# Performance work log

Measured on AMD Instinct MI355X. Metric: run time of the kernel, lower is better.

The kernel has to match this reference:

```python
import jax, jax.numpy as jnp
import numpy as np

N_T = 256
N_LAT = 1024
N_INN = 512
N_G = 512
N_MU = 64
N_NEU = 1024  # MLP hidden width (both MLP_p and MLP_m)
N_HID = 2     # hidden layers per MLP


def _linear(x, w, b=None):
    y = x @ w.T
    return y if b is None else y + b


def _mlp(x, in_w, in_b, h0_w, h0_b, h1_w, h1_b, out_w, out_b):
    f = jax.nn.leaky_relu(_linear(x, in_w, in_b))
    f = jax.nn.leaky_relu(_linear(f, h0_w, h0_b))
    f = jax.nn.leaky_relu(_linear(f, h1_w, h1_b))
    return _linear(f, out_w, out_b)


def setup_inputs() -> dict:
    key = jax.random.key(0)
    ks = jax.random.split(key, 24)

    def w(k, out_f, in_f):
        return jax.random.normal(k, (out_f, in_f), jnp.float32) / np.sqrt(in_f)

    def b(k, out_f):
        return jax.random.normal(k, (out_f,), jnp.float32) * 0.01

    return {
        "mu": jax.random.normal(ks[0], (N_MU,), jnp.float32),
        "z_0": jax.random.normal(ks[1], (N_LAT,), jnp.float32),
        # attention projections (no bias)
        "W1": w(ks[2], N_LAT, N_INN),
        "W2": w(ks[3], N_INN, N_LAT),
        "W3": w(ks[4], N_G, N_LAT),
        # MLP_p: N_MU -> N_NEU -> (x2) -> N_LAT
        "p_in_w": w(ks[5], N_NEU, N_MU), "p_in_b": b(ks[6], N_NEU),
        "p_h0_w": w(ks[7], N_NEU, N_NEU), "p_h0_b": b(ks[8], N_NEU),
        "p_h1_w": w(ks[9], N_NEU, N_NEU), "p_h1_b": b(ks[10], N_NEU),
        "p_out_w": w(ks[11], N_LAT, N_NEU), "p_out_b": b(ks[12], N_LAT),
        # MLP_m: N_G -> N_NEU -> (x2) -> N_LAT
        "m_in_w": w(ks[13], N_NEU, N_G), "m_in_b": b(ks[14], N_NEU),
        "m_h0_w": w(ks[15], N_NEU, N_NEU), "m_h0_b": b(ks[16], N_NEU),
        "m_h1_w": w(ks[17], N_NEU, N_NEU), "m_h1_b": b(ks[18], N_NEU),
        "m_out_w": w(ks[19], N_LAT, N_NEU), "m_out_b": b(ks[20], N_LAT),
    }


def reference(mu, z_0, W1, W2, W3,
              p_in_w, p_in_b, p_h0_w, p_h0_b, p_h1_w, p_h1_b, p_out_w, p_out_b,
              m_in_w, m_in_b, m_h0_w, m_h0_b, m_h1_w, m_h1_b, m_out_w, m_out_b):
    inv_sqrt = 1.0 / jnp.sqrt(jnp.asarray(N_LAT, jnp.float32))

    z_minus = _mlp(mu, p_in_w, p_in_b, p_h0_w, p_h0_b, p_h1_w, p_h1_b, p_out_w, p_out_b)
    Z0 = jnp.zeros((N_T + 1, N_LAT), mu.dtype).at[0].set(z_minus).at[1].set(z_0)

    def step(Z, t):
        # z_prev = Z[t-1]
        z_prev = jax.lax.dynamic_slice(Z, (t - 1, 0), (1, N_LAT))[0]
        # NOTE: faithful to the torch code -- attention over the FULL Z matrix,
        # including not-yet-filled zero rows (they contribute exp(0) to softmax).
        proj = (Z @ W2.T) @ W1.T                      # [N_t+1, N_lat]
        a = jax.nn.softmax(proj @ z_prev * inv_sqrt)  # [N_t+1]
        g = a @ (Z @ W3.T)                            # [N_g]
        z_new = z_prev + _mlp(g, m_in_w, m_in_b, m_h0_w, m_h0_b,
                              m_h1_w, m_h1_b, m_out_w, m_out_b)
        Z = jax.lax.dynamic_update_slice(Z, z_new[None, :], (t, 0))
        return Z, None

    Z_tilde, _ = jax.lax.scan(step, Z0, jnp.arange(2, N_T + 1))
    return Z_tilde
```

## Files before the change

kernel.cpp:

```cpp
#include <hip/hip_runtime.h>
#include <math.h>


#define NTHR 512
#define NBLK 256

#define B_AC   4096
#define B_SM   36864
#define B_C    102400
#define B_F    167936
#define B_ZM   233472
#define B_GC   299008
#define B_DV   315392

typedef int i4 __attribute__((ext_vector_type(4)));

__device__ __forceinline__ float i2f(int x) { return __int_as_float(x); }
__device__ __forceinline__ int f2i(float x) { return __float_as_int(x); }

__device__ __forceinline__ void astore(float* p, float v) {
  __hip_atomic_store(p, v, __ATOMIC_RELAXED, __HIP_MEMORY_SCOPE_AGENT);
}
__device__ __forceinline__ float2 aload2(const float* p) {
  double d = __hip_atomic_load((double*)p, __ATOMIC_RELAXED, __HIP_MEMORY_SCOPE_AGENT);
  return __builtin_bit_cast(float2, d);
}
__device__ __forceinline__ int aloadI(const int* p) {
  return __hip_atomic_load((int*)p, __ATOMIC_RELAXED, __HIP_MEMORY_SCOPE_AGENT);
}
__device__ __forceinline__ int afaddI(int* p) {
  return __hip_atomic_fetch_add(p, 1, __ATOMIC_RELAXED, __HIP_MEMORY_SCOPE_AGENT);
}

__device__ __forceinline__ i4 poll16(const i4* p, int tag) {
  i4 v;
  for (;;) {
    asm volatile("global_load_dwordx4 %0, %1, off sc0 sc1\n\ts_waitcnt vmcnt(0)"
                 : "=&v"(v) : "v"(p) : "memory");
    if (v.w == tag) return v;
    __builtin_amdgcn_s_sleep(1);
  }
}
__device__ __forceinline__ void store16(i4* p, i4 v) {
  asm volatile("global_store_dwordx4 %0, %1, off sc0 sc1" :: "v"(p), "v"(v) : "memory");
}

__device__ __forceinline__ float wred(float v) {
#pragma unroll
  for (int o = 1; o < 64; o <<= 1) v += __shfl_xor(v, o, 64);
  return v;
}
__device__ __forceinline__ void wred2(float& a, float& b) {
#pragma unroll
  for (int o = 1; o < 64; o <<= 1) { a += __shfl_xor(a, o, 64); b += __shfl_xor(b, o, 64); }
}
__device__ __forceinline__ void wred3(float& a, float& b, float& c) {
#pragma unroll
  for (int o = 1; o < 64; o <<= 1) {
    a += __shfl_xor(a, o, 64); b += __shfl_xor(b, o, 64); c += __shfl_xor(c, o, 64);
  }
}
__device__ __forceinline__ float wmax(float v) {
#pragma unroll
  for (int o = 1; o < 64; o <<= 1) v = fmaxf(v, __shfl_xor(v, o, 64));
  return v;
}
__device__ __forceinline__ float lrelu(float x) { return x > 0.f ? x : 0.01f * x; }

__device__ __forceinline__ void gsync1(int* bar, int bid, int tid, int lane) {
  asm volatile("" ::: "memory");
  __builtin_amdgcn_s_waitcnt(0);
  __syncthreads();
  if (tid == 0) afaddI(bar + (bid & 7) * 16);
  if (tid < 64) {
    for (;;) {
      int v = (lane < 8) ? aloadI(bar + lane * 16) : 0x7fffffff;
      if (__all(v >= 32)) break;
      __builtin_amdgcn_s_sleep(2);
    }
  }
  __syncthreads();
  asm volatile("" ::: "memory");
}

__global__ void __launch_bounds__(NTHR) tcell(
    const float* __restrict__ mu, const float* __restrict__ z0,
    const float* __restrict__ W1, const float* __restrict__ W2, const float* __restrict__ W3,
    const float* __restrict__ p_in_w, const float* __restrict__ p_in_b,
    const float* __restrict__ p_h0_w, const float* __restrict__ p_h0_b,
    const float* __restrict__ p_h1_w, const float* __restrict__ p_h1_b,
    const float* __restrict__ p_out_w, const float* __restrict__ p_out_b,
    const float* __restrict__ m_in_w, const float* __restrict__ m_in_b,
    const float* __restrict__ m_h0_w, const float* __restrict__ m_h0_b,
    const float* __restrict__ m_h1_w, const float* __restrict__ m_h1_b,
    const float* __restrict__ m_out_w, const float* __restrict__ m_out_b,
    float* __restrict__ Z, float* __restrict__ ws) {
  const int tid = threadIdx.x;
  const int bid = blockIdx.x;
  const int lane = tid & 63;
  const int wave = tid >> 6;
  const int r = 4 * bid + (wave & 3);
  const int rep = bid & 7;

  char* wsb = (char*)ws;
  int* bar = (int*)wsb;
  i4* aC  = (i4*)(wsb + B_AC);
  i4* smC = (i4*)(wsb + B_SM);
  i4* cCh = (i4*)(wsb + B_C);
  i4* fCh = (i4*)(wsb + B_F);
  i4* zmC = (i4*)(wsb + B_ZM);
  i4* gC  = (i4*)(wsb + B_GC);
  float* dVec = (float*)(wsb + B_DV);
  i4* aCr  = aC  + rep * 256;
  i4* smCr = smC + rep * 512;
  i4* cChr = cCh + rep * 512;
  i4* fChr = fCh + rep * 512;
  i4* zmCr = zmC + rep * 512;

  __shared__ float sX[1024], sDv[1024];
  __shared__ float sLg[256], sNp[256], sPp[256], sR[256];
  __shared__ float sBigB[4][1024], sBigW[4][1024];
  __shared__ float sU[4][257];
  __shared__ float shD[4], shDp[4], shZ[4], shG[4], shGv[4], shF[4];

  float4 rB4[4], rW4[4];
  if (wave < 4) {
#pragma unroll
    for (int q = 0; q < 4; ++q) {
      rB4[q] = make_float4(0.f, 0.f, 0.f, 0.f);
      rW4[q] = make_float4(0.f, 0.f, 0.f, 0.f);
    }
    const float* __restrict__ w1r = W1 + (size_t)r * 512;
    const float* __restrict__ mir = m_in_w + (size_t)r * 512;
    for (int k = 0; k < 512; k += 2) {
      float w1a = w1r[k], w1b = w1r[k + 1];
      float mia = mir[k], mib = mir[k + 1];
      const float* w2a = W2 + (size_t)k * 1024 + 4 * lane;
      const float* w3a = W3 + (size_t)k * 1024 + 4 * lane;
#pragma unroll
      for (int q = 0; q < 4; ++q) {
        float4 a0 = *(const float4*)(w2a + 256 * q);
        float4 a1 = *(const float4*)(w2a + 1024 + 256 * q);
        float4 b0 = *(const float4*)(w3a + 256 * q);
        float4 b1 = *(const float4*)(w3a + 1024 + 256 * q);
        rB4[q].x = fmaf(w1a, a0.x, fmaf(w1b, a1.x, rB4[q].x));
        rB4[q].y = fmaf(w1a, a0.y, fmaf(w1b, a1.y, rB4[q].y));
        rB4[q].z = fmaf(w1a, a0.z, fmaf(w1b, a1.z, rB4[q].z));
        rB4[q].w = fmaf(w1a, a0.w, fmaf(w1b, a1.w, rB4[q].w));
        rW4[q].x = fmaf(mia, b0.x, fmaf(mib, b1.x, rW4[q].x));
        rW4[q].y = fmaf(mia, b0.y, fmaf(mib, b1.y, rW4[q].y));
        rW4[q].z = fmaf(mia, b0.z, fmaf(mib, b1.z, rW4[q].z));
        rW4[q].w = fmaf(mia, b0.w, fmaf(mib, b1.w, rW4[q].w));
      }
    }
  } else if (wave == 4) {
    float f[4];
#pragma unroll
    for (int j = 0; j < 4; ++j) {
      int row = 4 * bid + j;
      float acc = p_in_w[(size_t)row * 64 + lane] * mu[lane];
      acc = wred(acc);
      f[j] = lrelu(acc + p_in_b[row]);
    }
    if (lane < 16) {
      int rp = lane >> 1, ch = lane & 1;
      i4 c; c.x = f2i(f[2 * ch]); c.y = f2i(f[2 * ch + 1]); c.z = 0; c.w = 1;
      store16(smC + rp * 512 + 2 * bid + ch, c);
    }
  }

#define MVP(WPTR, BPTR, ACT, INC, INTAG, OUTC, OUTTAG)                         \
  { i4 v = poll16((INC) + tid, (INTAG)); sX[2*tid] = i2f(v.x); sX[2*tid+1] = i2f(v.y); } \
  __syncthreads();                                                             \
  if (wave < 4) {                                                              \
    const float* w = (WPTR) + (size_t)r * 1024 + 4 * lane;                     \
    float acc = 0.f;                                                           \
    _Pragma("unroll")                                                          \
    for (int q = 0; q < 4; ++q) {                                              \
      float4 wf = *(const float4*)(w + 256 * q);                               \
      float4 xf = *(const float4*)(sX + 4 * lane + 256 * q);                   \
      acc = fmaf(wf.x, xf.x, acc); acc = fmaf(wf.y, xf.y, acc);                \
      acc = fmaf(wf.z, xf.z, acc); acc = fmaf(wf.w, xf.w, acc);                \
    }                                                                          \
    acc = wred(acc);                                                           \
    if (lane == 0) { float vv = acc + (BPTR)[r]; shF[wave] = (ACT) ? lrelu(vv) : vv; } \
  }                                                                            \
  __syncthreads();                                                             \
  if (tid < 16) {                                                              \
    int rp = tid >> 1, ch = tid & 1;                                           \
    i4 c; c.x = f2i(shF[2*ch]); c.y = f2i(shF[2*ch+1]); c.z = 0; c.w = (OUTTAG); \
    store16((OUTC) + rp * 512 + 2 * bid + ch, c);                              \
  }

  MVP(p_h0_w, p_h0_b, 1, smCr, 1, cCh, 1)
  MVP(p_h1_w, p_h1_b, 1, cChr, 1, fCh, 1)
  MVP(p_out_w, p_out_b, 0, fChr, 1, zmC, 1)
  if (tid == 16) *(float4*)(Z + 4 * bid) = make_float4(shF[0], shF[1], shF[2], shF[3]);
  if (bid < 2) Z[1024 + bid * 512 + tid] = z0[bid * 512 + tid];

  float d0_w = 0.f, d_prev = 0.f, z_prev = 0.f;
  { i4 v = poll16(zmCr + tid, 1); sDv[2*tid] = i2f(v.x); sDv[2*tid+1] = i2f(v.y); }
  { float2 a = *(const float2*)(z0 + 2 * tid); sX[2*tid] = a.x; sX[2*tid+1] = a.y; }
  __syncthreads();
  if (wave < 4) {
    float aD = 0.f, aU = 0.f, bD = 0.f, bU = 0.f;
#pragma unroll
    for (int q = 0; q < 4; ++q) {
      float4 zm = *(const float4*)(sDv + 4 * lane + 256 * q);
      float4 z1 = *(const float4*)(sX + 4 * lane + 256 * q);
      aD = fmaf(rB4[q].x, zm.x, aD); aD = fmaf(rB4[q].y, zm.y, aD);
      aD = fmaf(rB4[q].z, zm.z, aD); aD = fmaf(rB4[q].w, zm.w, aD);
      aU = fmaf(rW4[q].x, zm.x, aU); aU = fmaf(rW4[q].y, zm.y, aU);
      aU = fmaf(rW4[q].z, zm.z, aU); aU = fmaf(rW4[q].w, zm.w, aU);
      bD = fmaf(rB4[q].x, z1.x, bD); bD = fmaf(rB4[q].y, z1.y, bD);
      bD = fmaf(rB4[q].z, z1.z, bD); bD = fmaf(rB4[q].w, z1.w, bD);
      bU = fmaf(rW4[q].x, z1.x, bU); bU = fmaf(rW4[q].y, z1.y, bU);
      bU = fmaf(rW4[q].z, z1.z, bU); bU = fmaf(rW4[q].w, z1.w, bU);
    }
    wred2(aD, aU); wred2(bD, bU);
    d0_w = aD; d_prev = bD; z_prev = z0[r];
    if (lane == 0) {
      sU[wave][0] = aU; sU[wave][1] = bU;
      astore(dVec + 1024 + r, aD);
      astore(dVec + r, bD);
    }
  }
  gsync1(bar, bid, tid, lane);

  float4 rMT[4];
  if (wave < 4) {
#pragma unroll
    for (int q = 0; q < 4; ++q) {
      int m0 = 4 * lane + 256 * q;
      rMT[q].x = m_out_w[(size_t)(m0 + 0) * 1024 + r];
      rMT[q].y = m_out_w[(size_t)(m0 + 1) * 1024 + r];
      rMT[q].z = m_out_w[(size_t)(m0 + 2) * 1024 + r];
      rMT[q].w = m_out_w[(size_t)(m0 + 3) * 1024 + r];
    }
  }

  float lgreg = 0.f, dmob = 0.f;
  float4 G4 = make_float4(0.f, 0.f, 0.f, 0.f);

#define GWORK(PAR, TAG, ROWID)                                                 \
  { float2 a = aload2(dVec + (PAR) * 1024 + 2 * tid);                          \
    sDv[2*tid] = a.x; sDv[2*tid+1] = a.y; }                                    \
  __syncthreads();                                                             \
  if (wave < 4) {                                                              \
    float acc = 0.f;                                                           \
    _Pragma("unroll")                                                          \
    for (int q = 0; q < 4; ++q) {                                              \
      float4 d4 = *(const float4*)(sDv + 4 * lane + 256 * q);                  \
      acc = fmaf(rMT[q].x, d4.x, acc); acc = fmaf(rMT[q].y, d4.y, acc);        \
      acc = fmaf(rMT[q].z, d4.z, acc); acc = fmaf(rMT[q].w, d4.w, acc);        \
    }                                                                          \
    acc = wred(acc);                                                           \
    if (lane == 0) shGv[wave] = acc;                                           \
  }                                                                            \
  { float pd = sDv[tid] * m_out_b[tid] + sDv[tid+512] * m_out_b[tid+512];      \
    sX[tid] = pd; }                                                            \
  __syncthreads();                                                             \
  if (wave == 0) {                                                             \
    float s = sX[lane] + sX[lane+64] + sX[lane+128] + sX[lane+192]             \
            + sX[lane+256] + sX[lane+320] + sX[lane+384] + sX[lane+448];       \
    s = wred(s);                                                               \
    if (bid == (ROWID)) dmob = s;                                              \
    if (lane < 2) {                                                            \
      i4 c; c.x = f2i(shGv[2*lane]); c.y = f2i(shGv[2*lane+1]); c.z = 0;       \
      c.w = (TAG);                                                             \
      store16(gC + (PAR) * 512 + 2 * bid + lane, c);                           \
    }                                                                          \
  }

  GWORK(1, 1, 0)

  float4 rBM[4], rWM[4], rMo[4];
  float bmob = 0.f, wmob = 0.f, mob_own = 0.f;
  if (wave < 4) {
#pragma unroll
    for (int q = 0; q < 4; ++q) {
      *(float4*)(&sBigB[wave][4 * lane + 256 * q]) = rB4[q];
      *(float4*)(&sBigW[wave][4 * lane + 256 * q]) = rW4[q];
      rBM[q] = make_float4(0.f, 0.f, 0.f, 0.f);
      rWM[q] = make_float4(0.f, 0.f, 0.f, 0.f);
    }
  }
  __syncthreads();
  if (wave < 4) {
    for (int m = 0; m < 1024; ++m) {
      float bB = sBigB[wave][m], bW = sBigW[wave][m];
      float mb = m_out_b[m];
      bmob = fmaf(bB, mb, bmob); wmob = fmaf(bW, mb, wmob);
      const float* mo = m_out_w + (size_t)m * 1024 + 4 * lane;
#pragma unroll
      for (int q = 0; q < 4; ++q) {
        float4 m4 = *(const float4*)(mo + 256 * q);
        rBM[q].x = fmaf(bB, m4.x, rBM[q].x); rBM[q].y = fmaf(bB, m4.y, rBM[q].y);
        rBM[q].z = fmaf(bB, m4.z, rBM[q].z); rBM[q].w = fmaf(bB, m4.w, rBM[q].w);
        rWM[q].x = fmaf(bW, m4.x, rWM[q].x); rWM[q].y = fmaf(bW, m4.y, rWM[q].y);
        rWM[q].z = fmaf(bW, m4.z, rWM[q].z); rWM[q].w = fmaf(bW, m4.w, rWM[q].w);
      }
    }
#pragma unroll
    for (int q = 0; q < 4; ++q)
      rMo[q] = *(const float4*)(m_out_w + (size_t)r * 1024 + 4 * lane + 256 * q);
    mob_own = m_out_b[r];
  }

  for (int t = 2; t <= 256; ++t) {
    if (t == 2) {
      if (wave < 4 && lane == 0) { shD[wave] = d_prev; shDp[wave] = d0_w; shZ[wave] = z_prev; }
      __syncthreads();
    } else {
      { i4 v = poll16(fChr + tid, t - 1); sX[2*tid] = i2f(v.x); sX[2*tid+1] = i2f(v.y); }
      __syncthreads();
      if (wave < 4) {
        float dB = 0.f, dW = 0.f, dM = 0.f;
#pragma unroll
        for (int q = 0; q < 4; ++q) {
          float4 xf = *(const float4*)(sX + 4 * lane + 256 * q);
          dB = fmaf(rBM[q].x, xf.x, dB); dB = fmaf(rBM[q].y, xf.y, dB);
          dB = fmaf(rBM[q].z, xf.z, dB); dB = fmaf(rBM[q].w, xf.w, dB);
          dW = fmaf(rWM[q].x, xf.x, dW); dW = fmaf(rWM[q].y, xf.y, dW);
          dW = fmaf(rWM[q].z, xf.z, dW); dW = fmaf(rWM[q].w, xf.w, dW);
          dM = fmaf(rMo[q].x, xf.x, dM); dM = fmaf(rMo[q].y, xf.y, dM);
          dM = fmaf(rMo[q].z, xf.z, dM); dM = fmaf(rMo[q].w, xf.w, dM);
        }
        wred3(dB, dW, dM);
        float d_new = d_prev + dB + bmob;
        float U_new = sU[wave][t - 2] + dW + wmob;
        float z_new = z_prev + dM + mob_own;
        if (lane == 0) {
          sU[wave][t - 1] = U_new;
          astore(Z + (size_t)(t - 1) * 1024 + r, z_new);
          astore(dVec + (t & 1) * 1024 + r, d_new);
          shD[wave] = d_new; shDp[wave] = d_prev; shZ[wave] = z_new;
        }
        __builtin_amdgcn_s_waitcnt(0);
        d_prev = d_new; z_prev = z_new;
      } else {
        int u = tid - 256;
        float gp = G4.x * sX[4*u] + G4.y * sX[4*u+1] + G4.z * sX[4*u+2] + G4.w * sX[4*u+3];
        gp = wred(gp);
        if (lane == 0) shG[wave - 4] = gp;
      }
      __syncthreads();
    }
    if (wave == 0) {
      float np = shD[0]*shZ[0] + shD[1]*shZ[1] + shD[2]*shZ[2] + shD[3]*shZ[3];
      float pp = shDp[0]*shZ[0] + shDp[1]*shZ[1] + shDp[2]*shZ[2] + shDp[3]*shZ[3];
      if (t >= 3 && bid <= t - 3)
        lgreg += shG[0] + shG[1] + shG[2] + shG[3] + dmob;
      if (lane < 8) {
        i4 c; c.x = f2i(lgreg); c.y = f2i(np); c.z = f2i(pp); c.w = t;
        store16(aC + lane * 256 + bid, c);
      }
    }

    if (tid < 256) {
      i4 v = poll16(aCr + tid, t);
      sLg[tid] = i2f(v.x); sNp[tid] = i2f(v.y); sPp[tid] = i2f(v.z);
    }
    __syncthreads();
    if (wave == 0) {
      float ns = sNp[lane] + sNp[lane+64] + sNp[lane+128] + sNp[lane+192];
      float ps = sPp[lane] + sPp[lane+64] + sPp[lane+128] + sPp[lane+192];
      wred2(ns, ps);
      if (bid == t - 2) lgreg = ps;
      float l[4]; float mx = -1e30f;
#pragma unroll
      for (int j = 0; j < 4; ++j) {
        int i = lane + 64 * j;
        float li = -1e30f;
        if (i <= t - 3) li = sLg[i] * 0.03125f;
        else if (i == t - 2) li = ps * 0.03125f;
        else if (i == t - 1) li = ns * 0.03125f;
        l[j] = li; mx = fmaxf(mx, li);
      }
      mx = wmax(mx);
      float m = fmaxf(mx, 0.f);
      float e[4], es = 0.f;
#pragma unroll
      for (int j = 0; j < 4; ++j) {
        int i = lane + 64 * j;
        e[j] = (i <= t - 1) ? __expf(l[j] - m) : 0.f;
        es += e[j];
      }
      es = wred(es);
      float inv = 1.f / (es + (float)(257 - t) * __expf(-m));
#pragma unroll
      for (int j = 0; j < 4; ++j) sR[lane + 64 * j] = e[j] * inv;
    }
    __syncthreads();
    if (wave < 4) {
      float acc = 0.f;
#pragma unroll
      for (int j = 0; j < 4; ++j) {
        int i = lane + 64 * j;
        if (i <= t - 1) acc = fmaf(sR[i], sU[wave][i], acc);
      }
      acc = wred(acc);
      if (lane == 0) shF[wave] = lrelu(acc + m_in_b[r]);
    }
    __syncthreads();
    if (tid < 16) {
      int rp = tid >> 1, ch = tid & 1;
      i4 c; c.x = f2i(shF[2*ch]); c.y = f2i(shF[2*ch+1]); c.z = 0; c.w = t;
      store16(smC + rp * 512 + 2 * bid + ch, c);
    }

    MVP(m_h0_w, m_h0_b, 1, smCr, t, cCh, t)

    MVP(m_h1_w, m_h1_b, 1, cChr, t, fCh, t)

    if (t <= 254) {
      GWORK((t & 1), t, t - 1)
    }
    if (t == bid + 2 && bid <= 253) {
      if (tid >= 256) {
        int u = tid - 256;
        const i4* gbase = gC + ((bid + 1) & 1) * 512;
        i4 c0 = poll16(gbase + 2 * u, bid + 1);
        i4 c1 = poll16(gbase + 2 * u + 1, bid + 1);
        G4.x = i2f(c0.x); G4.y = i2f(c0.y); G4.z = i2f(c1.x); G4.w = i2f(c1.y);
      }
    }
  }

  { i4 v = poll16(fChr + tid, 256); sX[2*tid] = i2f(v.x); sX[2*tid+1] = i2f(v.y); }
  __syncthreads();
  if (wave < 4) {
    float dM = 0.f;
#pragma unroll
    for (int q = 0; q < 4; ++q) {
      float4 xf = *(const float4*)(sX + 4 * lane + 256 * q);
      dM = fmaf(rMo[q].x, xf.x, dM); dM = fmaf(rMo[q].y, xf.y, dM);
      dM = fmaf(rMo[q].z, xf.z, dM); dM = fmaf(rMo[q].w, xf.w, dM);
    }
    dM = wred(dM);
    if (lane == 0) astore(Z + (size_t)256 * 1024 + r, z_prev + dM + mob_own);
  }
}

extern "C" void kernel_launch(void* const* d_in, const int* in_sizes, int n_in,
                              void* d_out, int out_size, void* d_ws, size_t ws_size,
                              hipStream_t stream) {
  (void)in_sizes; (void)n_in; (void)out_size; (void)ws_size;
  hipMemsetAsync(d_ws, 0, 315392, stream);
  tcell<<<dim3(NBLK), dim3(NTHR), 0, stream>>>(
      (const float*)d_in[0],  (const float*)d_in[1],
      (const float*)d_in[2],  (const float*)d_in[3],  (const float*)d_in[4],
      (const float*)d_in[5],  (const float*)d_in[6],
      (const float*)d_in[7],  (const float*)d_in[8],
      (const float*)d_in[9],  (const float*)d_in[10],
      (const float*)d_in[11], (const float*)d_in[12],
      (const float*)d_in[13], (const float*)d_in[14],
      (const float*)d_in[15], (const float*)d_in[16],
      (const float*)d_in[17], (const float*)d_in[18],
      (const float*)d_in[19], (const float*)d_in[20],
      (float*)d_out, (float*)d_ws);
}
```

Measured before the change: 2.867 ms.

## Publish one value per tagged slot directly from each wave, dropping block barrier

Each wave now writes its own MLP output row straight to the 8 replicated exchange buffers, one float per tagged 16-byte slot. Before, the four wave results were gathered in shared memory behind a __syncthreads and packed two per slot. Consumers poll two slots per thread with both loads in flight. This removes one block-wide barrier per matrix-vector stage on the serial critical path, at the cost of doubling workspace size, memset bytes and polling traffic.

```diff
diff --git a/kernel.cpp b/kernel.cpp
--- a/kernel.cpp
+++ b/kernel.cpp
@@ -7,11 +7,11 @@
 
 #define B_AC   4096
 #define B_SM   36864
-#define B_C    102400
-#define B_F    167936
-#define B_ZM   233472
-#define B_GC   299008
-#define B_DV   315392
+#define B_C    167936
+#define B_F    299008
+#define B_ZM   430080
+#define B_GC   561152
+#define B_DV   577536
 
 typedef int i4 __attribute__((ext_vector_type(4)));
 
@@ -43,6 +43,23 @@
 }
 __device__ __forceinline__ void store16(i4* p, i4 v) {
   asm volatile("global_store_dwordx4 %0, %1, off sc0 sc1" :: "v"(p), "v"(v) : "memory");
+}
+__device__ __forceinline__ void pollf(const i4* base, int tag, int tid, float* dst) {
+  i4 a, b;
+  int got = 0;
+  for (;;) {
+    if (!(got & 1))
+      asm volatile("global_load_dwordx4 %0, %1, off sc0 sc1"
+                   : "=v"(a) : "v"(base + tid) : "memory");
+    if (!(got & 2))
+      asm volatile("global_load_dwordx4 %0, %1, off sc0 sc1"
+                   : "=v"(b) : "v"(base + tid + 512) : "memory");
+    asm volatile("s_waitcnt vmcnt(0)" ::: "memory");
+    if (!(got & 1) && a.w == tag) { got |= 1; dst[tid] = i2f(a.x); }
+    if (!(got & 2) && b.w == tag) { got |= 2; dst[tid + 512] = i2f(b.x); }
+    if (got == 3) return;
+    __builtin_amdgcn_s_sleep(1);
+  }
 }
 
 __device__ __forceinline__ float wred(float v) {
@@ -112,16 +129,16 @@
   i4* gC  = (i4*)(wsb + B_GC);
   float* dVec = (float*)(wsb + B_DV);
   i4* aCr  = aC  + rep * 256;
-  i4* smCr = smC + rep * 512;
-  i4* cChr = cCh + rep * 512;
-  i4* fChr = fCh + rep * 512;
-  i4* zmCr = zmC + rep * 512;
+  i4* smCr = smC + rep * 1024;
+  i4* cChr = cCh + rep * 1024;
+  i4* fChr = fCh + rep * 1024;
+  i4* zmCr = zmC + rep * 1024;
 
   __shared__ float sX[1024], sDv[1024];
   __shared__ float sLg[256], sNp[256], sPp[256], sR[256];
   __shared__ float sBigB[4][1024], sBigW[4][1024];
   __shared__ float sU[4][257];
-  __shared__ float shD[4], shDp[4], shZ[4], shG[4], shGv[4], shF[4];
+  __shared__ float shD[4], shDp[4], shZ[4], shG[4], shGv[4];
 
   float4 rB4[4], rW4[4];
   if (wave < 4) {
@@ -154,23 +171,21 @@
       }
     }
   } else if (wave == 4) {
-    float f[4];
 #pragma unroll
     for (int j = 0; j < 4; ++j) {
       int row = 4 * bid + j;
       float acc = p_in_w[(size_t)row * 64 + lane] * mu[lane];
       acc = wred(acc);
-      f[j] = lrelu(acc + p_in_b[row]);
-    }
-    if (lane < 16) {
-      int rp = lane >> 1, ch = lane & 1;
-      i4 c; c.x = f2i(f[2 * ch]); c.y = f2i(f[2 * ch + 1]); c.z = 0; c.w = 1;
-      store16(smC + rp * 512 + 2 * bid + ch, c);
+      float vv = lrelu(acc + p_in_b[row]);
+      if (lane < 8) {
+        i4 c; c.x = f2i(vv); c.y = 0; c.z = 0; c.w = 1;
+        store16(smC + lane * 1024 + row, c);
+      }
     }
   }
 
 #define MVP(WPTR, BPTR, ACT, INC, INTAG, OUTC, OUTTAG)                         \
-  { i4 v = poll16((INC) + tid, (INTAG)); sX[2*tid] = i2f(v.x); sX[2*tid+1] = i2f(v.y); } \
+  pollf((INC), (INTAG), tid, sX);                                              \
   __syncthreads();                                                             \
   if (wave < 4) {                                                              \
     const float* w = (WPTR) + (size_t)r * 1024 + 4 * lane;                     \
@@ -183,23 +198,40 @@
       acc = fmaf(wf.z, xf.z, acc); acc = fmaf(wf.w, xf.w, acc);                \
     }                                                                          \
     acc = wred(acc);                                                           \
-    if (lane == 0) { float vv = acc + (BPTR)[r]; shF[wave] = (ACT) ? lrelu(vv) : vv; } \
-  }                                                                            \
-  __syncthreads();                                                             \
-  if (tid < 16) {                                                              \
-    int rp = tid >> 1, ch = tid & 1;                                           \
-    i4 c; c.x = f2i(shF[2*ch]); c.y = f2i(shF[2*ch+1]); c.z = 0; c.w = (OUTTAG); \
-    store16((OUTC) + rp * 512 + 2 * bid + ch, c);                              \
+    float vv = acc + (BPTR)[r];                                                \
+    if (ACT) vv = lrelu(vv);                                                   \
+    if (lane < 8) {                                                            \
+      i4 c; c.x = f2i(vv); c.y = 0; c.z = 0; c.w = (OUTTAG);                   \
+      store16((OUTC) + lane * 1024 + r, c);                                    \
+    }                                                                          \
   }
 
   MVP(p_h0_w, p_h0_b, 1, smCr, 1, cCh, 1)
   MVP(p_h1_w, p_h1_b, 1, cChr, 1, fCh, 1)
-  MVP(p_out_w, p_out_b, 0, fChr, 1, zmC, 1)
-  if (tid == 16) *(float4*)(Z + 4 * bid) = make_float4(shF[0], shF[1], shF[2], shF[3]);
+  pollf(fChr, 1, tid, sX);
+  __syncthreads();
+  if (wave < 4) {
+    const float* w = p_out_w + (size_t)r * 1024 + 4 * lane;
+    float acc = 0.f;
+#pragma unroll
+    for (int q = 0; q < 4; ++q) {
+      float4 wf = *(const float4*)(w + 256 * q);
+      float4 xf = *(const float4*)(sX + 4 * lane + 256 * q);
+      acc = fmaf(wf.x, xf.x, acc); acc = fmaf(wf.y, xf.y, acc);
+      acc = fmaf(wf.z, xf.z, acc); acc = fmaf(wf.w, xf.w, acc);
+    }
+    acc = wred(acc);
+    float vv = acc + p_out_b[r];
+    if (lane < 8) {
+      i4 c; c.x = f2i(vv); c.y = 0; c.z = 0; c.w = 1;
+      store16(zmC + lane * 1024 + r, c);
+    }
+    if (lane == 8) astore(Z + r, vv);
+  }
   if (bid < 2) Z[1024 + bid * 512 + tid] = z0[bid * 512 + tid];
 
   float d0_w = 0.f, d_prev = 0.f, z_prev = 0.f;
-  { i4 v = poll16(zmCr + tid, 1); sDv[2*tid] = i2f(v.x); sDv[2*tid+1] = i2f(v.y); }
+  pollf(zmCr, 1, tid, sDv);
   { float2 a = *(const float2*)(z0 + 2 * tid); sX[2*tid] = a.x; sX[2*tid+1] = a.y; }
   __syncthreads();
   if (wave < 4) {
@@ -312,7 +344,7 @@
       if (wave < 4 && lane == 0) { shD[wave] = d_prev; shDp[wave] = d0_w; shZ[wave] = z_prev; }
       __syncthreads();
     } else {
-      { i4 v = poll16(fChr + tid, t - 1); sX[2*tid] = i2f(v.x); sX[2*tid+1] = i2f(v.y); }
+      pollf(fChr, t - 1, tid, sX);
       __syncthreads();
       if (wave < 4) {
         float dB = 0.f, dW = 0.f, dM = 0.f;
@@ -400,13 +432,11 @@
         if (i <= t - 1) acc = fmaf(sR[i], sU[wave][i], acc);
       }
       acc = wred(acc);
-      if (lane == 0) shF[wave] = lrelu(acc + m_in_b[r]);
-    }
-    __syncthreads();
-    if (tid < 16) {
-      int rp = tid >> 1, ch = tid & 1;
-      i4 c; c.x = f2i(shF[2*ch]); c.y = f2i(shF[2*ch+1]); c.z = 0; c.w = t;
-      store16(smC + rp * 512 + 2 * bid + ch, c);
+      float vv = lrelu(acc + m_in_b[r]);
+      if (lane < 8) {
+        i4 c; c.x = f2i(vv); c.y = 0; c.z = 0; c.w = t;
+        store16(smC + lane * 1024 + r, c);
+      }
     }
 
     MVP(m_h0_w, m_h0_b, 1, smCr, t, cCh, t)
@@ -427,7 +457,7 @@
     }
   }
 
-  { i4 v = poll16(fChr + tid, 256); sX[2*tid] = i2f(v.x); sX[2*tid+1] = i2f(v.y); }
+  pollf(fChr, 256, tid, sX);
   __syncthreads();
   if (wave < 4) {
     float dM = 0.f;
@@ -446,7 +476,7 @@
                               void* d_out, int out_size, void* d_ws, size_t ws_size,
                               hipStream_t stream) {
   (void)in_sizes; (void)n_in; (void)out_size; (void)ws_size;
-  hipMemsetAsync(d_ws, 0, 315392, stream);
+  hipMemsetAsync(d_ws, 0, 577536, stream);
   tcell<<<dim3(NBLK), dim3(NTHR), 0, stream>>>(
       (const float*)d_in[0],  (const float*)d_in[1],
       (const float*)d_in[2],  (const float*)d_in[3],  (const float*)d_in[4],
```

Result: slower. 3.519 ms (+22.7%).

## Remove per-layer block barriers by double-buffering shared input and two-row waves

Applied to the files above, without the earlier changes.

Each matvec layer now uses two waves that each compute two output rows and publish their chunks directly from lanes, instead of four waves writing to shared scratch followed by a barrier and a separate store. The shared input buffer alternates between two arrays so the next layer's fill does not race with the previous layer's reads. This drops one __syncthreads per MLP layer on the serial step-to-step critical path. The cost is that half as many waves issue the weight loads, so each wave carries twice the load and FMA latency, and an extra barrier is added on the final step.

```diff
diff --git a/kernel.cpp b/kernel.cpp
--- a/kernel.cpp
+++ b/kernel.cpp
@@ -117,11 +117,11 @@
   i4* fChr = fCh + rep * 512;
   i4* zmCr = zmC + rep * 512;
 
-  __shared__ float sX[1024], sDv[1024];
+  __shared__ float sXa[1024], sXb[1024], sDv[1024];
   __shared__ float sLg[256], sNp[256], sPp[256], sR[256];
   __shared__ float sBigB[4][1024], sBigW[4][1024];
   __shared__ float sU[4][257];
-  __shared__ float shD[4], shDp[4], shZ[4], shG[4], shGv[4], shF[4];
+  __shared__ float shD[4], shDp[4], shZ[4], shG[4], shGv[4];
 
   float4 rB4[4], rW4[4];
   if (wave < 4) {
@@ -169,45 +169,73 @@
     }
   }
 
-#define MVP(WPTR, BPTR, ACT, INC, INTAG, OUTC, OUTTAG)                         \
-  { i4 v = poll16((INC) + tid, (INTAG)); sX[2*tid] = i2f(v.x); sX[2*tid+1] = i2f(v.y); } \
+#define MVP(WPTR, BPTR, ACT, INC, INTAG, OUTC, OUTTAG, BUF)                    \
+  { i4 v = poll16((INC) + tid, (INTAG));                                       \
+    BUF[2*tid] = i2f(v.x); BUF[2*tid+1] = i2f(v.y); }                          \
   __syncthreads();                                                             \
-  if (wave < 4) {                                                              \
-    const float* w = (WPTR) + (size_t)r * 1024 + 4 * lane;                     \
-    float acc = 0.f;                                                           \
+  if (wave < 2) {                                                              \
+    int ra = 4 * bid + 2 * wave, rb = ra + 1;                                  \
+    const float* wa = (WPTR) + (size_t)ra * 1024 + 4 * lane;                   \
+    const float* wb = (WPTR) + (size_t)rb * 1024 + 4 * lane;                   \
+    float a0 = 0.f, a1 = 0.f;                                                  \
     _Pragma("unroll")                                                          \
     for (int q = 0; q < 4; ++q) {                                              \
-      float4 wf = *(const float4*)(w + 256 * q);                               \
-      float4 xf = *(const float4*)(sX + 4 * lane + 256 * q);                   \
-      acc = fmaf(wf.x, xf.x, acc); acc = fmaf(wf.y, xf.y, acc);                \
-      acc = fmaf(wf.z, xf.z, acc); acc = fmaf(wf.w, xf.w, acc);                \
+      float4 xf = *(const float4*)(BUF + 4 * lane + 256 * q);                  \
+      float4 w0 = *(const float4*)(wa + 256 * q);                              \
+      float4 w1 = *(const float4*)(wb + 256 * q);                              \
+      a0 = fmaf(w0.x, xf.x, a0); a0 = fmaf(w0.y, xf.y, a0);                    \
+      a0 = fmaf(w0.z, xf.z, a0); a0 = fmaf(w0.w, xf.w, a0);                    \
+      a1 = fmaf(w1.x, xf.x, a1); a1 = fmaf(w1.y, xf.y, a1);                    \
+      a1 = fmaf(w1.z, xf.z, a1); a1 = fmaf(w1.w, xf.w, a1);                    \
     }                                                                          \
-    acc = wred(acc);                                                           \
-    if (lane == 0) { float vv = acc + (BPTR)[r]; shF[wave] = (ACT) ? lrelu(vv) : vv; } \
-  }                                                                            \
-  __syncthreads();                                                             \
-  if (tid < 16) {                                                              \
-    int rp = tid >> 1, ch = tid & 1;                                           \
-    i4 c; c.x = f2i(shF[2*ch]); c.y = f2i(shF[2*ch+1]); c.z = 0; c.w = (OUTTAG); \
-    store16((OUTC) + rp * 512 + 2 * bid + ch, c);                              \
-  }
-
-  MVP(p_h0_w, p_h0_b, 1, smCr, 1, cCh, 1)
-  MVP(p_h1_w, p_h1_b, 1, cChr, 1, fCh, 1)
-  MVP(p_out_w, p_out_b, 0, fChr, 1, zmC, 1)
-  if (tid == 16) *(float4*)(Z + 4 * bid) = make_float4(shF[0], shF[1], shF[2], shF[3]);
+    wred2(a0, a1);                                                             \
+    float v0 = a0 + (BPTR)[ra], v1 = a1 + (BPTR)[rb];                          \
+    if (ACT) { v0 = lrelu(v0); v1 = lrelu(v1); }                               \
+    if (lane < 8) {                                                            \
+      i4 c; c.x = f2i(v0); c.y = f2i(v1); c.z = 0; c.w = (OUTTAG);             \
+      store16((OUTC) + lane * 512 + 2 * bid + wave, c);                        \
+    }                                                                          \
+  }
+
+  MVP(p_h0_w, p_h0_b, 1, smCr, 1, cCh, 1, sXb)
+  MVP(p_h1_w, p_h1_b, 1, cChr, 1, fCh, 1, sXa)
+  { i4 v = poll16(fChr + tid, 1); sXb[2*tid] = i2f(v.x); sXb[2*tid+1] = i2f(v.y); }
+  __syncthreads();
+  if (wave < 2) {
+    int ra = 4 * bid + 2 * wave, rb = ra + 1;
+    const float* wa = p_out_w + (size_t)ra * 1024 + 4 * lane;
+    const float* wb = p_out_w + (size_t)rb * 1024 + 4 * lane;
+    float a0 = 0.f, a1 = 0.f;
+#pragma unroll
+    for (int q = 0; q < 4; ++q) {
+      float4 xf = *(const float4*)(sXb + 4 * lane + 256 * q);
+      float4 w0 = *(const float4*)(wa + 256 * q);
+      float4 w1 = *(const float4*)(wb + 256 * q);
+      a0 = fmaf(w0.x, xf.x, a0); a0 = fmaf(w0.y, xf.y, a0);
+      a0 = fmaf(w0.z, xf.z, a0); a0 = fmaf(w0.w, xf.w, a0);
+      a1 = fmaf(w1.x, xf.x, a1); a1 = fmaf(w1.y, xf.y, a1);
+      a1 = fmaf(w1.z, xf.z, a1); a1 = fmaf(w1.w, xf.w, a1);
+    }
+    wred2(a0, a1);
+    float v0 = a0 + p_out_b[ra], v1 = a1 + p_out_b[rb];
+    if (lane < 8) {
+      i4 c; c.x = f2i(v0); c.y = f2i(v1); c.z = 0; c.w = 1;
+      store16(zmC + lane * 512 + 2 * bid + wave, c);
+    }
+    if (lane == 8) { astore(Z + ra, v0); astore(Z + rb, v1); }
+  }
   if (bid < 2) Z[1024 + bid * 512 + tid] = z0[bid * 512 + tid];
 
   float d0_w = 0.f, d_prev = 0.f, z_prev = 0.f;
   { i4 v = poll16(zmCr + tid, 1); sDv[2*tid] = i2f(v.x); sDv[2*tid+1] = i2f(v.y); }
-  { float2 a = *(const float2*)(z0 + 2 * tid); sX[2*tid] = a.x; sX[2*tid+1] = a.y; }
+  { float2 a = *(const float2*)(z0 + 2 * tid); sXa[2*tid] = a.x; sXa[2*tid+1] = a.y; }
   __syncthreads();
   if (wave < 4) {
     float aD = 0.f, aU = 0.f, bD = 0.f, bU = 0.f;
 #pragma unroll
     for (int q = 0; q < 4; ++q) {
       float4 zm = *(const float4*)(sDv + 4 * lane + 256 * q);
-      float4 z1 = *(const float4*)(sX + 4 * lane + 256 * q);
+      float4 z1 = *(const float4*)(sXa + 4 * lane + 256 * q);
       aD = fmaf(rB4[q].x, zm.x, aD); aD = fmaf(rB4[q].y, zm.y, aD);
       aD = fmaf(rB4[q].z, zm.z, aD); aD = fmaf(rB4[q].w, zm.w, aD);
       aU = fmaf(rW4[q].x, zm.x, aU); aU = fmaf(rW4[q].y, zm.y, aU);
@@ -258,11 +286,11 @@
     if (lane == 0) shGv[wave] = acc;                                           \
   }                                                                            \
   { float pd = sDv[tid] * m_out_b[tid] + sDv[tid+512] * m_out_b[tid+512];      \
-    sX[tid] = pd; }                                                            \
+    sXb[tid] = pd; }                                                           \
   __syncthreads();                                                             \
   if (wave == 0) {                                                             \
-    float s = sX[lane] + sX[lane+64] + sX[lane+128] + sX[lane+192]             \
-            + sX[lane+256] + sX[lane+320] + sX[lane+384] + sX[lane+448];       \
+    float s = sXb[lane] + sXb[lane+64] + sXb[lane+128] + sXb[lane+192]         \
+            + sXb[lane+256] + sXb[lane+320] + sXb[lane+384] + sXb[lane+448];   \
     s = wred(s);                                                               \
     if (bid == (ROWID)) dmob = s;                                              \
     if (lane < 2) {                                                            \
@@ -312,13 +340,13 @@
       if (wave < 4 && lane == 0) { shD[wave] = d_prev; shDp[wave] = d0_w; shZ[wave] = z_prev; }
       __syncthreads();
     } else {
-      { i4 v = poll16(fChr + tid, t - 1); sX[2*tid] = i2f(v.x); sX[2*tid+1] = i2f(v.y); }
+      { i4 v = poll16(fChr + tid, t - 1); sXa[2*tid] = i2f(v.x); sXa[2*tid+1] = i2f(v.y); }
       __syncthreads();
       if (wave < 4) {
         float dB = 0.f, dW = 0.f, dM = 0.f;
 #pragma unroll
         for (int q = 0; q < 4; ++q) {
-          float4 xf = *(const float4*)(sX + 4 * lane + 256 * q);
+          float4 xf = *(const float4*)(sXa + 4 * lane + 256 * q);
           dB = fmaf(rBM[q].x, xf.x, dB); dB = fmaf(rBM[q].y, xf.y, dB);
           dB = fmaf(rBM[q].z, xf.z, dB); dB = fmaf(rBM[q].w, xf.w, dB);
           dW = fmaf(rWM[q].x, xf.x, dW); dW = fmaf(rWM[q].y, xf.y, dW);
@@ -340,7 +368,7 @@
         d_prev = d_new; z_prev = z_new;
       } else {
         int u = tid - 256;
-        float gp = G4.x * sX[4*u] + G4.y * sX[4*u+1] + G4.z * sX[4*u+2] + G4.w * sX[4*u+3];
+        float gp = G4.x * sXa[4*u] + G4.y * sXa[4*u+1] + G4.z * sXa[4*u+2] + G4.w * sXa[4*u+3];
         gp = wred(gp);
         if (lane == 0) shG[wave - 4] = gp;
       }
@@ -392,29 +420,35 @@
       for (int j = 0; j < 4; ++j) sR[lane + 64 * j] = e[j] * inv;
     }
     __syncthreads();
-    if (wave < 4) {
-      float acc = 0.f;
+    if (wave < 2) {
+      int ra = 4 * bid + 2 * wave;
+      float a0 = 0.f, a1 = 0.f;
 #pragma unroll
       for (int j = 0; j < 4; ++j) {
         int i = lane + 64 * j;
-        if (i <= t - 1) acc = fmaf(sR[i], sU[wave][i], acc);
-      }
-      acc = wred(acc);
-      if (lane == 0) shF[wave] = lrelu(acc + m_in_b[r]);
-    }
-    __syncthreads();
-    if (tid < 16) {
-      int rp = tid >> 1, ch = tid & 1;
-      i4 c; c.x = f2i(shF[2*ch]); c.y = f2i(shF[2*ch+1]); c.z = 0; c.w = t;
-      store16(smC + rp * 512 + 2 * bid + ch, c);
-    }
-
-    MVP(m_h0_w, m_h0_b, 1, smCr, t, cCh, t)
-
-    MVP(m_h1_w, m_h1_b, 1, cChr, t, fCh, t)
+        if (i <= t - 1) {
+          float av = sR[i];
+          a0 = fmaf(av, sU[2 * wave][i], a0);
+          a1 = fmaf(av, sU[2 * wave + 1][i], a1);
+        }
+      }
+      wred2(a0, a1);
+      float v0 = lrelu(a0 + m_in_b[ra]);
+      float v1 = lrelu(a1 + m_in_b[ra + 1]);
+      if (lane < 8) {
+        i4 c; c.x = f2i(v0); c.y = f2i(v1); c.z = 0; c.w = t;
+        store16(smC + lane * 512 + 2 * bid + wave, c);
+      }
+    }
+
+    MVP(m_h0_w, m_h0_b, 1, smCr, t, cCh, t, sXb)
+
+    MVP(m_h1_w, m_h1_b, 1, cChr, t, fCh, t, sXa)
 
     if (t <= 254) {
       GWORK((t & 1), t, t - 1)
+    } else {
+      __syncthreads();
     }
     if (t == bid + 2 && bid <= 253) {
       if (tid >= 256) {
@@ -427,13 +461,13 @@
     }
   }
 
-  { i4 v = poll16(fChr + tid, 256); sX[2*tid] = i2f(v.x); sX[2*tid+1] = i2f(v.y); }
+  { i4 v = poll16(fChr + tid, 256); sXa[2*tid] = i2f(v.x); sXa[2*tid+1] = i2f(v.y); }
   __syncthreads();
   if (wave < 4) {
     float dM = 0.f;
 #pragma unroll
     for (int q = 0; q < 4; ++q) {
-      float4 xf = *(const float4*)(sX + 4 * lane + 256 * q);
+      float4 xf = *(const float4*)(sXa + 4 * lane + 256 * q);
       dM = fmaf(rMo[q].x, xf.x, dM); dM = fmaf(rMo[q].y, xf.y, dM);
       dM = fmaf(rMo[q].z, xf.z, dM); dM = fmaf(rMo[q].w, xf.w, dM);
     }
```

New measurement: 3.189 ms. +11.2%, slower.
